# Optimization experiments

Hardware: AMD Instinct MI355X
Metric: run time of the kernel (lower is better)

The kernel has to match this reference:

```python
import jax, jax.numpy as jnp
import numpy as np

NH = 32          # num_attention_heads
LAYER_ID = 3     # per-layer scaling coeff = LAYER_ID + 1
SQ, B, H = 1024, 2, 4096
MEM_LEN = 1024
HD = H // NH


def setup_inputs() -> dict:
    key = jax.random.key(0)
    ks = jax.random.split(key, 6)
    hidden_states = jax.random.normal(ks[0], (SQ, B, H), dtype=jnp.float32)
    mem = jax.random.normal(ks[1], (B, MEM_LEN, 2 * NH * HD), dtype=jnp.float32) * 0.5
    qkv_w = jax.random.normal(ks[2], (3 * H, H), dtype=jnp.float32) * 0.02
    qkv_b = jax.random.normal(ks[3], (3 * H,), dtype=jnp.float32) * 0.02
    dense_w = jax.random.normal(ks[4], (H, H), dtype=jnp.float32) * 0.02
    dense_b = jax.random.normal(ks[5], (H,), dtype=jnp.float32) * 0.02
    # causal mask over new tokens; mem positions fully visible. True = masked.
    kv = MEM_LEN + SQ
    mask = ((jnp.arange(kv)[None, :] - MEM_LEN) > jnp.arange(SQ)[:, None])
    mask = mask[None, None, :, :]  # [1,1,sq,kv]
    # position ids of new tokens continue after the mem cache: [b, sq]
    position_ids = jnp.broadcast_to(MEM_LEN + jnp.arange(SQ, dtype=jnp.int64), (B, SQ))
    return {"hidden_states": hidden_states, "mask": mask, "position_ids": position_ids,
            "mem": mem, "qkv_w": qkv_w, "qkv_b": qkv_b, "dense_w": dense_w, "dense_b": dense_b}


def _rotate_half(x):
    x1, x2 = jnp.split(x, 2, axis=-1)
    return jnp.concatenate((-x2, x1), axis=-1)


def _rotary_tables(max_pos):
    inv_freq = 1.0 / (10000.0 ** (jnp.arange(0, HD, 2, dtype=jnp.float32) / HD))
    t = jnp.arange(max_pos, dtype=jnp.float32)
    freqs = jnp.einsum('i,j->ij', t, inv_freq)          # [L, HD/2]
    emb = jnp.concatenate((freqs, freqs), axis=-1)      # [L, HD]
    return jnp.cos(emb), jnp.sin(emb)


def reference(hidden_states, mask, position_ids, mem, qkv_w, qkv_b, dense_w, dense_b):
    sq, b, h = hidden_states.shape
    coeff = float(LAYER_ID + 1)
    # QKV projection: [sq,b,3H] -> [sq,b,nh,3*hd] -> split
    mixed = jnp.einsum('sbh,oh->sbo', hidden_states, qkv_w) + qkv_b
    mixed = mixed.reshape(sq, b, NH, 3 * HD)
    q, k, v = jnp.split(mixed, 3, axis=-1)              # each [sq,b,nh,hd]
    # rotary embedding with position indices (position_ids: [b,sq] -> [sq,b])
    pos = position_ids.T                                 # [sq,b]
    cos_t, sin_t = _rotary_tables(MEM_LEN + SQ)          # table up to max pos + 1
    cos = cos_t[pos][:, :, None, :]                      # [sq,b,1,hd]
    sin = sin_t[pos][:, :, None, :]
    q = q * cos + _rotate_half(q) * sin
    k = k * cos + _rotate_half(k) * sin
    # mem-KV concat: mem [b, mem_len, 2*nh*hd] -> memk/memv [mem_len,b,nh,hd]
    m = mem.reshape(b, MEM_LEN, 2, NH, HD).transpose(2, 1, 0, 3, 4)
    k = jnp.concatenate((m[0], k), axis=0)               # [kv,b,nh,hd]
    v = jnp.concatenate((m[1], v), axis=0)
    # per-layer scaled attention scores
    q = q / (np.sqrt(HD) * coeff)
    scores = jnp.einsum('sbnh,tbnh->bnst', q, k)         # [b,nh,sq,kv]
    scores = jnp.where(mask, -10000.0, scores)
    scores = scores * coeff
    probs = jax.nn.softmax(scores, axis=-1)
    ctx = jnp.einsum('bnst,tbnh->sbnh', probs, v).reshape(sq, b, h)
    out = jnp.einsum('sbh,oh->sbo', ctx, dense_w) + dense_b
    return out
```

## Files before the change

### kernel.cpp

```cpp
#include <hip/hip_runtime.h>


typedef __attribute__((ext_vector_type(4))) float f32x4;
typedef __attribute__((ext_vector_type(8))) short bf16x8;
typedef unsigned short u16;

#define SQ   1024
#define BSZ  2
#define H    4096
#define NH   32
#define HD   128
#define MEML 1024
#define KV   2048

__device__ __forceinline__ u16 f32_to_bf16(float f) {
  union { float f; unsigned int u; } v; v.f = f;
  unsigned int r = v.u + 0x7FFFu + ((v.u >> 16) & 1u);
  return (u16)(r >> 16);
}
__device__ __forceinline__ float bf16_to_f32(u16 x) {
  union { unsigned int u; float f; } v; v.u = ((unsigned int)x) << 16; return v.f;
}

__device__ __forceinline__ void gload_lds16(const void* g, void* l) {
  __builtin_amdgcn_global_load_lds((const __attribute__((address_space(1))) void*)g,
                                   (__attribute__((address_space(3))) void*)l, 16, 0, 0);
}

__global__ __launch_bounds__(256) void conv_bf16(const float* __restrict__ in,
                                                 u16* __restrict__ out, int n4) {
  int idx = blockIdx.x * 256 + threadIdx.x;
  if (idx < n4) {
    float4 v = ((const float4*)in)[idx];
    ushort4 o;
    o.x = f32_to_bf16(v.x); o.y = f32_to_bf16(v.y);
    o.z = f32_to_bf16(v.z); o.w = f32_to_bf16(v.w);
    ((ushort4*)out)[idx] = o;
  }
}

#define NA4 2097152
#define NB4 12582912
__global__ __launch_bounds__(256) void conv2(const float* __restrict__ a, u16* __restrict__ oa,
                                             const float* __restrict__ bsrc, u16* __restrict__ ob) {
  int idx = blockIdx.x * 256 + threadIdx.x;
  const float* s; u16* o; int off;
  if (idx < NA4) { s = a;    o = oa; off = idx; }
  else           { s = bsrc; o = ob; off = idx - NA4; }
  float4 v = ((const float4*)s)[off];
  ushort4 r;
  r.x = f32_to_bf16(v.x); r.y = f32_to_bf16(v.y);
  r.z = f32_to_bf16(v.z); r.w = f32_to_bf16(v.w);
  ((ushort4*)o)[off] = r;
}

__global__ __launch_bounds__(256) void rope_tables(float* __restrict__ cost, float* __restrict__ sint) {
  int idx = blockIdx.x * 256 + threadIdx.x;
  int s = idx >> 6, j = idx & 63;
  float inv = powf(10000.0f, -(float)j / 64.0f);
  float ang = (float)(MEML + s) * inv;
  cost[idx] = cosf(ang);
  sint[idx] = sinf(ang);
}

template <typename OUT_T, int NF>
__global__ __launch_bounds__(512, 2) void gemmT(const u16* __restrict__ A, const u16* __restrict__ B,
                                                const float* __restrict__ bias, OUT_T* __restrict__ C,
                                                int N, int K) {
  constexpr int WN = NF * 16;
  constexpr int NH0 = (NF + 1) / 2;
  constexpr int SB2 = NF - (NF >> 1);
  __shared__ char lds[2][32768 + NF * 8192];
  const int tid = threadIdx.x;
  const int lane = tid & 63;
  const int w = tid >> 6;
  const int wm = w >> 2, wn = w & 3;
  const int rl = lane & 15, cg = lane >> 4;
  const int m0 = blockIdx.y * 256, n0 = blockIdx.x * (NF * 64);
  const int nt = K >> 6;

  const int srow = tid >> 3;
  const int scb = ((tid & 7) << 4) ^ ((srow & 7) << 4);

  auto stage_a = [&](int tile, int ua) {
    if (tile >= nt) return;
    gload_lds16((const char*)(A + (size_t)(m0 + ua * 64 + srow) * K + (size_t)tile * 64) + scb,
                lds[tile & 1] + ua * 8192 + tid * 16);
  };
  auto stage_b = [&](int tile, int ub) {
    if (tile >= nt) return;
    gload_lds16((const char*)(B + (size_t)(n0 + ub * 64 + srow) * K + (size_t)tile * 64) + scb,
                lds[tile & 1] + 32768 + ub * 8192 + tid * 16);
  };

  f32x4 acc[8][NF];
#pragma unroll
  for (int i = 0; i < 8; ++i)
#pragma unroll
    for (int j = 0; j < NF; ++j) acc[i][j] = (f32x4){0.f, 0.f, 0.f, 0.f};

  bf16x8 af[4][2], bf[NF][2];

  auto read_a = [&](const char* buf, int mh) {
#pragma unroll
    for (int mi = 0; mi < 4; ++mi) {
      int R = wm * 128 + mh * 64 + mi * 16 + rl;
#pragma unroll
      for (int kk = 0; kk < 2; ++kk) {
        int cb = (kk * 64 + cg * 16) ^ ((R & 7) << 4);
        af[mi][kk] = *(const bf16x8*)(buf + R * 128 + cb);
      }
    }
  };
  auto read_b1 = [&](const char* buf, int nl) {
    int R = wn * WN + nl * 16 + rl;
#pragma unroll
    for (int kk = 0; kk < 2; ++kk) {
      int cb = (kk * 64 + cg * 16) ^ ((R & 7) << 4);
      bf[nl][kk] = *(const bf16x8*)(buf + 32768 + R * 128 + cb);
    }
  };
  auto mfset = [&](int mh, int lo, int hi) {
    __builtin_amdgcn_s_setprio(1);
#pragma unroll
    for (int kk = 0; kk < 2; ++kk)
#pragma unroll
      for (int mi = 0; mi < 4; ++mi)
#pragma unroll
        for (int nl = 0; nl < NF; ++nl)
          if (nl >= lo && nl < hi)
            acc[mh * 4 + mi][nl] = __builtin_amdgcn_mfma_f32_16x16x32_bf16(
                af[mi][kk], bf[nl][kk], acc[mh * 4 + mi][nl], 0, 0, 0);
    __builtin_amdgcn_s_setprio(0);
  };

#pragma unroll
  for (int ua = 0; ua < 4; ++ua) stage_a(0, ua);
#pragma unroll
  for (int ub = 0; ub < NF; ++ub) stage_b(0, ub);
#pragma unroll
  for (int ub = 0; ub < NF; ++ub) stage_b(1, ub);
  if (NF == 2)      { asm volatile("s_waitcnt vmcnt(2)" ::: "memory"); }
  else if (NF == 3) { asm volatile("s_waitcnt vmcnt(3)" ::: "memory"); }
  else              { asm volatile("s_waitcnt vmcnt(4)" ::: "memory"); }
  __builtin_amdgcn_s_barrier();

  for (int kt = 0; kt < nt; ++kt) {
    const char* buf = lds[kt & 1];
    read_a(buf, 0);
#pragma unroll
    for (int nl = 0; nl < NH0; ++nl) read_b1(buf, nl);
    stage_a(kt + 1, 0); stage_a(kt + 1, 1);
    __builtin_amdgcn_s_barrier();
    asm volatile("s_waitcnt lgkmcnt(0)" ::: "memory");
    mfset(0, 0, NH0);
    __builtin_amdgcn_s_barrier();
#pragma unroll
    for (int nl = NH0; nl < NF; ++nl) read_b1(buf, nl);
    stage_a(kt + 1, 2); stage_a(kt + 1, 3);
    __builtin_amdgcn_s_barrier();
    asm volatile("s_waitcnt lgkmcnt(0)" ::: "memory");
    mfset(0, NH0, NF);
    __builtin_amdgcn_s_barrier();
    read_a(buf, 1);
#pragma unroll
    for (int ub = 0; ub < SB2; ++ub) stage_b(kt + 2, ub);
    __builtin_amdgcn_s_barrier();
    asm volatile("s_waitcnt lgkmcnt(0)" ::: "memory");
    mfset(1, NH0, NF);
    __builtin_amdgcn_s_barrier();
#pragma unroll
    for (int ub = SB2; ub < NF; ++ub) stage_b(kt + 2, ub);
    __builtin_amdgcn_s_barrier();
    mfset(1, 0, NH0);
    if (kt + 2 < nt) {
      if (NF == 2)      { asm volatile("s_waitcnt vmcnt(2)" ::: "memory"); }
      else if (NF == 3) { asm volatile("s_waitcnt vmcnt(3)" ::: "memory"); }
      else              { asm volatile("s_waitcnt vmcnt(4)" ::: "memory"); }
    } else if (kt + 1 < nt) {
      asm volatile("s_waitcnt vmcnt(0)" ::: "memory");
    }
    __builtin_amdgcn_s_barrier();
  }

#pragma unroll
  for (int ni = 0; ni < NF; ++ni) {
    int col = n0 + wn * WN + ni * 16 + rl;
    float bv = bias[col];
#pragma unroll
    for (int mi = 0; mi < 8; ++mi) {
      int rbase = m0 + wm * 128 + mi * 16 + cg * 4;
#pragma unroll
      for (int j = 0; j < 4; ++j) {
        float v = acc[mi][ni][j] + bv;
        if constexpr (sizeof(OUT_T) == 2)
          C[(size_t)(rbase + j) * N + col] = (OUT_T)f32_to_bf16(v);
        else
          C[(size_t)(rbase + j) * N + col] = (OUT_T)v;
      }
    }
  }
}

__global__ __launch_bounds__(256) void prep_qk(const u16* __restrict__ mixed,
                                               const float* __restrict__ cost,
                                               const float* __restrict__ sint,
                                               u16* __restrict__ Qb, u16* __restrict__ Kb) {
  int s0 = blockIdx.x * 64, head = blockIdx.y;
  int b = head >> 5, nh = head & 31;
  int tid = threadIdx.x;
  const float qs = 0.08838834764831845f;
#pragma unroll
  for (int i = 0; i < 4; ++i) {
    int flat = i * 256 + tid;
    int sl = flat >> 4, jg = (flat & 15) << 2;
    int s = s0 + sl;
    size_t base = ((size_t)(s * 2 + b)) * 12288 + (size_t)nh * 384;
    ushort4 q1v = *(const ushort4*)(mixed + base + jg);
    ushort4 q2v = *(const ushort4*)(mixed + base + 64 + jg);
    ushort4 k1v = *(const ushort4*)(mixed + base + 128 + jg);
    ushort4 k2v = *(const ushort4*)(mixed + base + 192 + jg);
    float4 cv = *(const float4*)(cost + s * 64 + jg);
    float4 sv = *(const float4*)(sint + s * 64 + jg);
    const u16* q1a = (const u16*)&q1v; const u16* q2a = (const u16*)&q2v;
    const u16* k1a = (const u16*)&k1v; const u16* k2a = (const u16*)&k2v;
    const float* ca = (const float*)&cv; const float* sa = (const float*)&sv;
    ushort4 qo1, qo2, ko1, ko2;
    u16* qo1a = (u16*)&qo1; u16* qo2a = (u16*)&qo2;
    u16* ko1a = (u16*)&ko1; u16* ko2a = (u16*)&ko2;
#pragma unroll
    for (int e = 0; e < 4; ++e) {
      float q1 = bf16_to_f32(q1a[e]), q2 = bf16_to_f32(q2a[e]);
      float k1 = bf16_to_f32(k1a[e]), k2 = bf16_to_f32(k2a[e]);
      float c = ca[e], sn = sa[e];
      qo1a[e] = f32_to_bf16((q1 * c - q2 * sn) * qs);
      qo2a[e] = f32_to_bf16((q2 * c + q1 * sn) * qs);
      ko1a[e] = f32_to_bf16(k1 * c - k2 * sn);
      ko2a[e] = f32_to_bf16(k2 * c + k1 * sn);
    }
    size_t qoff = ((size_t)head * SQ + s) * HD;
    *(ushort4*)(Qb + qoff + jg)      = qo1;
    *(ushort4*)(Qb + qoff + 64 + jg) = qo2;
    size_t koff = ((size_t)head * KV + MEML + s) * HD;
    *(ushort4*)(Kb + koff + jg)      = ko1;
    *(ushort4*)(Kb + koff + 64 + jg) = ko2;
  }
}

__global__ __launch_bounds__(256) void prep_kv(const u16* __restrict__ mixed,
                                               const float* __restrict__ mem,
                                               u16* __restrict__ Kb, u16* __restrict__ Vtb) {
  int t0 = blockIdx.x * 64, head = blockIdx.y;
  int b = head >> 5, nh = head & 31;
  __shared__ u16 vt[128 * 72];
  int tid = threadIdx.x;
  if (t0 < MEML) {
#pragma unroll
    for (int i = 0; i < 8; ++i) {
      int flat = i * 256 + tid;
      int tl = flat >> 5, dg = (flat & 31) << 2;
      float4 kv4 = *(const float4*)(mem + ((size_t)b * MEML + t0 + tl) * 8192 + (size_t)nh * HD + dg);
      ushort4 o;
      o.x = f32_to_bf16(kv4.x); o.y = f32_to_bf16(kv4.y);
      o.z = f32_to_bf16(kv4.z); o.w = f32_to_bf16(kv4.w);
      *(ushort4*)(Kb + ((size_t)head * KV + t0 + tl) * HD + dg) = o;
    }
  }
#pragma unroll
  for (int i = 0; i < 8; ++i) {
    int flat = i * 256 + tid;
    int tl = flat >> 5, dg = (flat & 31) << 2;
    int t = t0 + tl;
    u16 e0, e1, e2, e3;
    if (t < MEML) {
      float4 v4 = *(const float4*)(mem + ((size_t)b * MEML + t) * 8192 + 4096 + (size_t)nh * HD + dg);
      e0 = f32_to_bf16(v4.x); e1 = f32_to_bf16(v4.y);
      e2 = f32_to_bf16(v4.z); e3 = f32_to_bf16(v4.w);
    } else {
      ushort4 v4 = *(const ushort4*)(mixed + ((size_t)((t - MEML) * 2 + b)) * 12288 + (size_t)nh * 384 + 256 + dg);
      e0 = v4.x; e1 = v4.y; e2 = v4.z; e3 = v4.w;
    }
    vt[(dg + 0) * 72 + tl] = e0;
    vt[(dg + 1) * 72 + tl] = e1;
    vt[(dg + 2) * 72 + tl] = e2;
    vt[(dg + 3) * 72 + tl] = e3;
  }
  __syncthreads();
#pragma unroll
  for (int i = 0; i < 4; ++i) {
    int c = i * 256 + tid;
    int d = c >> 3, slot = c & 7;
    *(bf16x8*)(Vtb + ((size_t)head * HD + d) * KV + t0 + slot * 8) =
        *(const bf16x8*)(vt + d * 72 + slot * 8);
  }
}

__global__ __launch_bounds__(512) void attn_fwd(const u16* __restrict__ Qb, const u16* __restrict__ Kb,
                                                const u16* __restrict__ Vtb, u16* __restrict__ ctx) {
  __shared__ u16 Ks[2][64 * 128];
  __shared__ u16 Vts[2][128 * 64];
  __shared__ u16 Ps[8 * 16 * 64];
  const int tid = threadIdx.x;
  const int lane = tid & 63;
  const int w = tid >> 6;
  const int q0 = blockIdx.x * 128;
  const int head = blockIdx.y;
  const int rl = lane & 15, cg = lane >> 4;
  const int sglob = q0 + w * 16 + rl;

  bf16x8 qf[4];
  {
    const u16* Qrow = Qb + ((size_t)head * SQ + sglob) * HD;
#pragma unroll
    for (int kk = 0; kk < 4; ++kk)
      qf[kk] = *(const bf16x8*)(Qrow + kk * 32 + cg * 8);
  }

  f32x4 acc[8];
#pragma unroll
  for (int i = 0; i < 8; ++i) acc[i] = (f32x4){0.f, 0.f, 0.f, 0.f};
  float mrow = -3.0e38f;
  float lrow = 0.f;

  const int ntile = (MEML + q0 + 128) >> 6;

  auto stageKV = [&](int it) {
    int t0 = it * 64;
    int buf = it & 1;
#pragma unroll
    for (int i = 0; i < 2; ++i) {
      int flat = i * 512 + tid;
      int row = flat >> 4;
      int scb = ((flat & 15) << 4) ^ ((row & 7) << 4);
      gload_lds16((const char*)(Kb + ((size_t)head * KV + t0 + row) * HD) + scb,
                  (char*)Ks[buf] + (flat << 4));
    }
#pragma unroll
    for (int i = 0; i < 2; ++i) {
      int flat = i * 512 + tid;
      int row = flat >> 3;
      int scb = ((flat & 7) << 4) ^ ((row & 7) << 4);
      gload_lds16((const char*)(Vtb + ((size_t)head * HD + row) * KV + t0) + scb,
                  (char*)Vts[buf] + (flat << 4));
    }
  };

  stageKV(0);

  for (int it = 0; it < ntile; ++it) {
    const int t0 = it * 64;
    if (it + 1 < ntile) {
      stageKV(it + 1);
      asm volatile("s_waitcnt vmcnt(4)" ::: "memory");
    } else {
      asm volatile("s_waitcnt vmcnt(0)" ::: "memory");
    }
    __builtin_amdgcn_s_barrier();
    const char* Kbuf = (const char*)Ks[it & 1];
    const char* Vbuf = (const char*)Vts[it & 1];
    const bool live = (t0 - MEML) <= (q0 + w * 16 + 15);
    if (live) {
      f32x4 sf[4];
#pragma unroll
      for (int tn = 0; tn < 4; ++tn) {
        f32x4 s = (f32x4){0.f, 0.f, 0.f, 0.f};
#pragma unroll
        for (int kk = 0; kk < 4; ++kk) {
          int row = tn * 16 + rl;
          int cb = (kk * 64 + cg * 16) ^ ((row & 7) << 4);
          bf16x8 kf = *(const bf16x8*)(Kbuf + row * 256 + cb);
          s = __builtin_amdgcn_mfma_f32_16x16x32_bf16(kf, qf[kk], s, 0, 0, 0);
        }
        sf[tn] = s;
      }
      if (t0 + 63 > MEML + q0 + w * 16) {
#pragma unroll
        for (int tn = 0; tn < 4; ++tn)
#pragma unroll
          for (int j = 0; j < 4; ++j) {
            int t = t0 + tn * 16 + cg * 4 + j;
            if (t - MEML > sglob) sf[tn][j] = -40000.0f;
          }
      }
      float mt = sf[0][0];
#pragma unroll
      for (int tn = 0; tn < 4; ++tn)
#pragma unroll
        for (int j = 0; j < 4; ++j) mt = fmaxf(mt, sf[tn][j]);
      mt = fmaxf(mt, __shfl_xor(mt, 16, 64));
      mt = fmaxf(mt, __shfl_xor(mt, 32, 64));
      float mn = fmaxf(mrow, mt);
      float psc = __expf(mrow - mn);
      mrow = mn;
      float ls = 0.f;
#pragma unroll
      for (int tn = 0; tn < 4; ++tn) {
        ushort4 pk;
        u16* pka = (u16*)&pk;
#pragma unroll
        for (int j = 0; j < 4; ++j) {
          float p = __expf(sf[tn][j] - mn);
          ls += p;
          pka[j] = f32_to_bf16(p);
        }
        int addr = w * 2048 + rl * 128 + ((tn * 32 + cg * 8) ^ ((rl & 7) << 4));
        *(ushort4*)((char*)Ps + addr) = pk;
      }
      ls += __shfl_xor(ls, 16, 64);
      ls += __shfl_xor(ls, 32, 64);
      lrow = lrow * psc + ls;
#pragma unroll
      for (int dn = 0; dn < 8; ++dn)
#pragma unroll
        for (int j = 0; j < 4; ++j) acc[dn][j] *= psc;
#pragma unroll
      for (int dn = 0; dn < 8; ++dn) {
#pragma unroll
        for (int kk2 = 0; kk2 < 2; ++kk2) {
          int pcb = (kk2 * 64 + cg * 16) ^ ((rl & 7) << 4);
          bf16x8 pf = *(const bf16x8*)((const char*)Ps + w * 2048 + rl * 128 + pcb);
          int vrow = dn * 16 + rl;
          int vcb = (kk2 * 64 + cg * 16) ^ ((vrow & 7) << 4);
          bf16x8 vf = *(const bf16x8*)(Vbuf + vrow * 128 + vcb);
          acc[dn] = __builtin_amdgcn_mfma_f32_16x16x32_bf16(vf, pf, acc[dn], 0, 0, 0);
        }
      }
    }
    __builtin_amdgcn_s_barrier();
  }

  const float inv = 1.0f / lrow;
  u16* T = (u16*)Ks;
  {
    int trow = w * 16 + rl;
#pragma unroll
    for (int dn = 0; dn < 8; ++dn) {
      ushort4 pk;
      u16* pka = (u16*)&pk;
#pragma unroll
      for (int j = 0; j < 4; ++j) pka[j] = f32_to_bf16(acc[dn][j] * inv);
      int addr = trow * 256 + ((dn * 32 + cg * 8) ^ ((rl & 7) << 4));
      *(ushort4*)((char*)T + addr) = pk;
    }
  }
  asm volatile("s_waitcnt lgkmcnt(0)" ::: "memory");
  __builtin_amdgcn_s_barrier();
  const int b = head >> 5, nh = head & 31;
#pragma unroll
  for (int i = 0; i < 4; ++i) {
    int flat = i * 512 + tid;
    int r = flat >> 4, c = flat & 15;
    bf16x8 v = *(const bf16x8*)((const char*)T + r * 256 + ((c * 16) ^ ((r & 7) << 4)));
    *(bf16x8*)(ctx + ((size_t)((q0 + r) * 2 + b)) * H + (size_t)nh * HD + c * 8) = v;
  }
}

extern "C" void kernel_launch(void* const* d_in, const int* in_sizes, int n_in,
                              void* d_out, int out_size, void* d_ws, size_t ws_size,
                              hipStream_t stream) {
  const float* hidden  = (const float*)d_in[0];
  const float* mem     = (const float*)d_in[3];
  const float* qkv_w   = (const float*)d_in[4];
  const float* qkv_b   = (const float*)d_in[5];
  const float* dense_w = (const float*)d_in[6];
  const float* dense_b = (const float*)d_in[7];
  float* out = (float*)d_out;
  char* ws = (char*)d_ws;

  u16* mixed = (u16*)ws;
  char* R1 = ws + 100663296;
  u16* hid_bf = (u16*)R1;
  u16* qw_bf  = (u16*)(R1 + 16777216);
  u16* Qb  = (u16*)R1;
  u16* Kb  = (u16*)(R1 + 16777216);
  u16* Vtb = (u16*)(R1 + 50331648);
  u16* ctx = (u16*)(R1 + 83886080);
  u16* dw_bf = (u16*)(R1 + 100663296);
  float* cost = (float*)(ws + 234881024);
  float* sint = (float*)(ws + 234881024 + 262144);

  conv2<<<57344, 256, 0, stream>>>(hidden, hid_bf, qkv_w, qw_bf);
  rope_tables<<<256, 256, 0, stream>>>(cost, sint);
  gemmT<u16, 3><<<dim3(64, 8), 512, 0, stream>>>(hid_bf, qw_bf, qkv_b, mixed, 12288, 4096);
  conv_bf16<<<16384, 256, 0, stream>>>(dense_w, dw_bf, 4194304);
  prep_qk<<<dim3(16, 64), 256, 0, stream>>>(mixed, cost, sint, Qb, Kb);
  prep_kv<<<dim3(32, 64), 256, 0, stream>>>(mixed, mem, Kb, Vtb);
  attn_fwd<<<dim3(8, 64), 512, 0, stream>>>(Qb, Kb, Vtb, ctx);
  gemmT<float, 2><<<dim3(32, 8), 512, 0, stream>>>(ctx, dw_bf, dense_b, out, 4096, 4096);
}
```

Before: 487.5 us.

## Split QKV GEMM into two tile-shape launches and fuse dense weight conversion

The dense-weight bf16 conversion is folded into the existing combined conversion kernel, so the separate conv kernel launch goes away. The QKV projection GEMM changes from one 64x8 grid with 192-wide N tiles into two launches. The first covers N columns 0-8191 with 256-wide tiles and the second covers 8192-12287 with 128-wide tiles, using a new n_base offset. Each launch has 256 blocks, matching the CU count, which is meant to improve wave quantization and per-tile reuse. The cost is an extra kernel launch and a possibly higher register footprint for NF=4.

After: 492.7 us. Within noise of the previous version (+1.1%).

```diff
diff --git a/kernel.cpp b/kernel.cpp
--- a/kernel.cpp
+++ b/kernel.cpp
@@ -27,26 +27,17 @@
                                    (__attribute__((address_space(3))) void*)l, 16, 0, 0);
 }
 
-__global__ __launch_bounds__(256) void conv_bf16(const float* __restrict__ in,
-                                                 u16* __restrict__ out, int n4) {
-  int idx = blockIdx.x * 256 + threadIdx.x;
-  if (idx < n4) {
-    float4 v = ((const float4*)in)[idx];
-    ushort4 o;
-    o.x = f32_to_bf16(v.x); o.y = f32_to_bf16(v.y);
-    o.z = f32_to_bf16(v.z); o.w = f32_to_bf16(v.w);
-    ((ushort4*)out)[idx] = o;
-  }
-}
-
 #define NA4 2097152
 #define NB4 12582912
-__global__ __launch_bounds__(256) void conv2(const float* __restrict__ a, u16* __restrict__ oa,
-                                             const float* __restrict__ bsrc, u16* __restrict__ ob) {
+#define NC4 4194304
+__global__ __launch_bounds__(256) void conv3(const float* __restrict__ a, u16* __restrict__ oa,
+                                             const float* __restrict__ bsrc, u16* __restrict__ ob,
+                                             const float* __restrict__ csrc, u16* __restrict__ oc) {
   int idx = blockIdx.x * 256 + threadIdx.x;
   const float* s; u16* o; int off;
-  if (idx < NA4) { s = a;    o = oa; off = idx; }
-  else           { s = bsrc; o = ob; off = idx - NA4; }
+  if (idx < NA4)            { s = a;    o = oa; off = idx; }
+  else if (idx < NA4 + NB4) { s = bsrc; o = ob; off = idx - NA4; }
+  else                      { s = csrc; o = oc; off = idx - (NA4 + NB4); }
   float4 v = ((const float4*)s)[off];
   ushort4 r;
   r.x = f32_to_bf16(v.x); r.y = f32_to_bf16(v.y);
@@ -66,7 +57,7 @@
 template <typename OUT_T, int NF>
 __global__ __launch_bounds__(512, 2) void gemmT(const u16* __restrict__ A, const u16* __restrict__ B,
                                                 const float* __restrict__ bias, OUT_T* __restrict__ C,
-                                                int N, int K) {
+                                                int N, int K, int n_base) {
   constexpr int WN = NF * 16;
   constexpr int NH0 = (NF + 1) / 2;
   constexpr int SB2 = NF - (NF >> 1);
@@ -76,7 +67,7 @@
   const int w = tid >> 6;
   const int wm = w >> 2, wn = w & 3;
   const int rl = lane & 15, cg = lane >> 4;
-  const int m0 = blockIdx.y * 256, n0 = blockIdx.x * (NF * 64);
+  const int m0 = blockIdx.y * 256, n0 = n_base + blockIdx.x * (NF * 64);
   const int nt = K >> 6;
 
   const int srow = tid >> 3;
@@ -468,6 +459,7 @@
   char* ws = (char*)d_ws;
 
   u16* mixed = (u16*)ws;
+  u16* dw_bf = (u16*)(ws + 50331648);
   char* R1 = ws + 100663296;
   u16* hid_bf = (u16*)R1;
   u16* qw_bf  = (u16*)(R1 + 16777216);
@@ -475,16 +467,15 @@
   u16* Kb  = (u16*)(R1 + 16777216);
   u16* Vtb = (u16*)(R1 + 50331648);
   u16* ctx = (u16*)(R1 + 83886080);
-  u16* dw_bf = (u16*)(R1 + 100663296);
   float* cost = (float*)(ws + 234881024);
   float* sint = (float*)(ws + 234881024 + 262144);
 
-  conv2<<<57344, 256, 0, stream>>>(hidden, hid_bf, qkv_w, qw_bf);
+  conv3<<<73728, 256, 0, stream>>>(hidden, hid_bf, qkv_w, qw_bf, dense_w, dw_bf);
   rope_tables<<<256, 256, 0, stream>>>(cost, sint);
-  gemmT<u16, 3><<<dim3(64, 8), 512, 0, stream>>>(hid_bf, qw_bf, qkv_b, mixed, 12288, 4096);
-  conv_bf16<<<16384, 256, 0, stream>>>(dense_w, dw_bf, 4194304);
+  gemmT<u16, 4><<<dim3(32, 8), 512, 0, stream>>>(hid_bf, qw_bf, qkv_b, mixed, 12288, 4096, 0);
+  gemmT<u16, 2><<<dim3(32, 8), 512, 0, stream>>>(hid_bf, qw_bf, qkv_b, mixed, 12288, 4096, 8192);
   prep_qk<<<dim3(16, 64), 256, 0, stream>>>(mixed, cost, sint, Qb, Kb);
   prep_kv<<<dim3(32, 64), 256, 0, stream>>>(mixed, mem, Kb, Vtb);
   attn_fwd<<<dim3(8, 64), 512, 0, stream>>>(Qb, Kb, Vtb, ctx);
-  gemmT<float, 2><<<dim3(32, 8), 512, 0, stream>>>(ctx, dw_bf, dense_b, out, 4096, 4096);
-}
+  gemmT<float, 2><<<dim3(32, 8), 512, 0, stream>>>(ctx, dw_bf, dense_b, out, 4096, 4096, 0);
+}
```
